# Performance work log

Measured on AMD Instinct MI355X. Metric: run time of the kernel, lower is better.

## Reference

```python
import jax, jax.numpy as jnp
import numpy as np

EMB = 1024
HEADS = 16
FFN = 4096
EPS = 1e-5


def _layernorm(x, g, b):
    mu = jnp.mean(x, axis=-1, keepdims=True)
    var = jnp.mean((x - mu) ** 2, axis=-1, keepdims=True)
    return (x - mu) * jax.lax.rsqrt(var + EPS) * g + b


def setup_inputs() -> dict:
    key = jax.random.key(0)
    ks = jax.random.split(key, 8)
    B, T = 2, 2048
    s_in = 1.0 / np.sqrt(EMB)
    s_ffn = 1.0 / np.sqrt(FFN)
    return {
        "x": jax.random.normal(ks[0], (B, T, EMB), jnp.float32),
        "positions": jnp.arange(B * T, dtype=jnp.int64 if jax.config.jax_enable_x64 else jnp.int32).reshape(B, T),
        "ln1_g": jnp.ones((EMB,), jnp.float32),
        "ln1_b": jnp.zeros((EMB,), jnp.float32),
        "ln2_g": jnp.ones((EMB,), jnp.float32),
        "ln2_b": jnp.zeros((EMB,), jnp.float32),
        "Wq": jax.random.normal(ks[1], (EMB, EMB), jnp.float32) * s_in,
        "bq": jnp.zeros((EMB,), jnp.float32),
        "Wk": jax.random.normal(ks[2], (EMB, EMB), jnp.float32) * s_in,
        "bk": jnp.zeros((EMB,), jnp.float32),
        "Wv": jax.random.normal(ks[3], (EMB, EMB), jnp.float32) * s_in,
        "bv": jnp.zeros((EMB,), jnp.float32),
        "Wo": jax.random.normal(ks[4], (EMB, EMB), jnp.float32) * s_in,
        "bo": jnp.zeros((EMB,), jnp.float32),
        "W1": jax.random.normal(ks[5], (EMB, FFN), jnp.float32) * s_in,
        "b1": jnp.zeros((FFN,), jnp.float32),
        "W2": jax.random.normal(ks[6], (FFN, EMB), jnp.float32) * s_ffn,
        "b2": jnp.zeros((EMB,), jnp.float32),
    }


def reference(x, positions, ln1_g, ln1_b, ln2_g, ln2_b,
              Wq, bq, Wk, bk, Wv, bv, Wo, bo, W1, b1, W2, b2):
    B, T, C = x.shape
    H, D = HEADS, C // HEADS
    # x = ln1(x); then residual branches add onto the normalized x (as in source)
    x = _layernorm(x, ln1_g, ln1_b)
    # --- self attention (rope=None, mask=None, dropout inactive) ---
    q = (x @ Wq + bq).reshape(B, T, H, D).transpose(0, 2, 1, 3)  # [B,H,T,D]
    k = (x @ Wk + bk).reshape(B, T, H, D).transpose(0, 2, 1, 3)
    v = (x @ Wv + bv).reshape(B, T, H, D).transpose(0, 2, 1, 3)
    scale = 1.0 / jnp.sqrt(jnp.asarray(D, x.dtype))
    attn = jnp.einsum("bhtd,bhsd->bhts", q, k) * scale  # [B,H,T,T]
    attn = jax.nn.softmax(attn, axis=-1)
    attn_out = jnp.einsum("bhts,bhsd->bhtd", attn, v)
    attn_out = attn_out.transpose(0, 2, 1, 3).reshape(B, T, C)
    attn_out = attn_out @ Wo + bo
    x = x + attn_out
    # --- FFN with exact (erf) GELU, matching torch nn.GELU default ---
    h = _layernorm(x, ln2_g, ln2_b)
    h = jax.nn.gelu(h @ W1 + b1, approximate=False)
    h = h @ W2 + b2
    return x + h
```

## Files before the change

### kernel.cpp

```cpp
#include <hip/hip_runtime.h>
#include <cstdint>
#include <cstddef>

typedef __bf16 bf16;
typedef __bf16 bf16x8 __attribute__((ext_vector_type(8)));
typedef __bf16 bf16x4 __attribute__((ext_vector_type(4)));
typedef float f32x4 __attribute__((ext_vector_type(4)));

#define TOKENS 4096
#define TSEQ   2048
#define NHEADS 16
#define HDIM   64
#define CDIM   1024

typedef __attribute__((address_space(3))) unsigned int lds_uint;
typedef __attribute__((address_space(1))) const unsigned int g_uint;
__device__ __forceinline__ void glds16(const bf16* g, bf16* l) {
  __builtin_amdgcn_global_load_lds((g_uint*)g, (lds_uint*)l, 16, 0, 0);
}

__device__ __forceinline__ float gelu_f(float v) {
  float g2 = v * (1.5957691216f + 0.0713548163f * v * v);
  return v / (1.0f + __expf(-g2));
}

#define NBUF 17
struct DetectArgs { const void* p[NBUF]; int n[NBUF]; };

__global__ __launch_bounds__(256) void detect_kernel(DetectArgs a, int* __restrict__ flags) {
  __shared__ int s_nz, s_bl;
  if (threadIdx.x == 0) { s_nz = 0; s_bl = 0; }
  __syncthreads();
  int i = blockIdx.x;
  const unsigned int* w = (const unsigned int*)a.p[i];
  int nwords = a.n[i] / 2; if (nwords > 2048) nwords = 2048;
  int nz = 0, bl = 0;
  for (int j = threadIdx.x; j < nwords; j += 256) {
    unsigned int v = w[j];
    if (v != 0u) {
      nz++;
      unsigned int e = (v >> 7) & 0xFFu;
      if (e >= 100u && e <= 140u) bl++;
    }
  }
  atomicAdd(&s_nz, nz);
  atomicAdd(&s_bl, bl);
  __syncthreads();
  if (threadIdx.x == 0) flags[i] = (2 * s_bl >= s_nz) ? 1 : 0;
}

__device__ __forceinline__ float ld_any(const void* p, size_t idx, bool isb) {
  return isb ? (float)((const bf16*)p)[idx] : ((const float*)p)[idx];
}

__device__ __forceinline__ void ln_stats(float s, float s2, int tid, float& mu, float& rstd) {
#pragma unroll
  for (int off = 32; off; off >>= 1) {
    s  += __shfl_down(s, off);
    s2 += __shfl_down(s2, off);
  }
  __shared__ float red[8];
  int w = tid >> 6;
  if ((tid & 63) == 0) { red[w] = s; red[4 + w] = s2; }
  __syncthreads();
  if (tid == 0) {
    red[0] = red[0] + red[1] + red[2] + red[3];
    red[4] = red[4] + red[5] + red[6] + red[7];
  }
  __syncthreads();
  mu = red[0] * (1.0f / CDIM);
  float var = fmaxf(red[4] * (1.0f / CDIM) - mu * mu, 0.f);
  rstd = rsqrtf(var + 1e-5f);
}

__global__ __launch_bounds__(256) void ln_f32(const float* __restrict__ x,
                                              const bf16* __restrict__ g,
                                              const bf16* __restrict__ b,
                                              bf16* __restrict__ y) {
  int row = blockIdx.x, tid = threadIdx.x;
  float v[4]; float s = 0.f, s2 = 0.f;
#pragma unroll
  for (int i = 0; i < 4; i++) {
    float f = x[(size_t)row * CDIM + tid * 4 + i];
    v[i] = f; s += f; s2 += f * f;
  }
  float mu, rstd;
  ln_stats(s, s2, tid, mu, rstd);
  bf16* yr = y + (size_t)row * CDIM;
#pragma unroll
  for (int i = 0; i < 4; i++) {
    int c = tid * 4 + i;
    yr[c] = (bf16)((v[i] - mu) * rstd * (float)g[c] + (float)b[c]);
  }
}

struct MegaArgs {
  const void* w_in[6]; bf16* w_out[6]; int wK[6], wN[6], wflag[6];
  const void* vp[10]; bf16* vd[10]; int vn[10], vfi[10];
  const void* x; const void* graw; const void* braw; bf16* y;
};

__global__ __launch_bounds__(256) void mega_pre(MegaArgs a, const int* __restrict__ flags) {
  int bid = blockIdx.x;
  int tx = threadIdx.x, ty = threadIdx.y;
  int tid = tx + ty * 64;
  if (bid < 3072) {
    __shared__ bf16 tile[64][65];
    int mi, start;
    if (bid < 1024)      { mi = bid >> 8; start = mi << 8; }
    else if (bid < 2048) { mi = 4; start = 1024; }
    else                 { mi = 5; start = 2048; }
    int tb = bid - start;
    int nT = a.wN[mi] >> 6;
    int kb = (tb / nT) * 64, nb = (tb % nT) * 64;
    int K = a.wK[mi], N = a.wN[mi];
    bool isb = flags[a.wflag[mi]] != 0;
    const void* in = a.w_in[mi]; bf16* out = a.w_out[mi];
    for (int i = ty; i < 64; i += 4)
      tile[i][tx] = (bf16)ld_any(in, (size_t)(kb + i) * N + nb + tx, isb);
    __syncthreads();
    for (int i = ty; i < 64; i += 4)
      out[(size_t)(nb + i) * K + kb + tx] = tile[tx][i];
  } else if (bid == 3072) {
    for (int i = 0; i < 10; i++) {
      bool isb = flags[a.vfi[i]] != 0;
      const void* in = a.vp[i]; bf16* out = a.vd[i]; int n = a.vn[i];
      for (int j = tid; j < n; j += 256)
        out[j] = (bf16)ld_any(in, j, isb);
    }
  } else {
    int row = bid - 3073;
    bool isb  = flags[0] != 0;
    bool gisb = flags[1] != 0;
    bool bisb = flags[2] != 0;
    float v[4]; float s = 0.f, s2 = 0.f;
#pragma unroll
    for (int i = 0; i < 4; i++) {
      float f = ld_any(a.x, (size_t)row * CDIM + tid * 4 + i, isb);
      v[i] = f; s += f; s2 += f * f;
    }
    float mu, rstd;
    ln_stats(s, s2, tid, mu, rstd);
    bf16* yr = a.y + (size_t)row * CDIM;
#pragma unroll
    for (int i = 0; i < 4; i++) {
      int c = tid * 4 + i;
      float gv = ld_any(a.graw, c, gisb);
      float bv = ld_any(a.braw, c, bisb);
      yr[c] = (bf16)((v[i] - mu) * rstd * gv + bv);
    }
  }
}

template <int BM, int BN>
__device__ __forceinline__ void gemm_core(const bf16* __restrict__ A,
                                          const bf16* __restrict__ Bt,
                                          int K, int m0, int n0,
                                          bf16* As, bf16* Bs,
                                          f32x4 (&acc)[BM / 32][BN / 32]) {
  constexpr int SI = BM / 32, SJ = BN / 32;
  int t = threadIdx.x;
  int wave = t >> 6, lane = t & 63, quad = lane >> 4, l16 = lane & 15;
  int wm = (wave & 1) * (BM / 2), wn = (wave >> 1) * (BN / 2);
  int srow = t >> 2, sc = t & 3;
  int swz = (srow >> 1) & 3;
  const bf16* ga[BM / 64];
  const bf16* gb[BN / 64];
#pragma unroll
  for (int h = 0; h < BM / 64; h++)
    ga[h] = A + (size_t)(m0 + h * 64 + srow) * K + (sc ^ swz) * 8;
#pragma unroll
  for (int h = 0; h < BN / 64; h++)
    gb[h] = Bt + (size_t)(n0 + h * 64 + srow) * K + (sc ^ swz) * 8;

  for (int k0 = 0; k0 < K; k0 += 64) {
#pragma unroll
    for (int q = 0; q < 2; q++) {
#pragma unroll
      for (int h = 0; h < BM / 64; h++)
        glds16(ga[h] + k0 + q * 32, As + q * (BM * 32) + h * 2048 + srow * 32 + sc * 8);
#pragma unroll
      for (int h = 0; h < BN / 64; h++)
        glds16(gb[h] + k0 + q * 32, Bs + q * (BN * 32) + h * 2048 + srow * 32 + sc * 8);
    }
    __syncthreads();
#pragma unroll
    for (int q = 0; q < 2; q++) {
      bf16x8 af[SI], bfr[SJ];
#pragma unroll
      for (int i = 0; i < SI; i++) {
        int m = wm + i * 16 + l16;
        af[i] = *(const bf16x8*)&As[q * (BM * 32) + m * 32 + ((quad ^ ((m >> 1) & 3)) * 8)];
      }
#pragma unroll
      for (int j = 0; j < SJ; j++) {
        int n = wn + j * 16 + l16;
        bfr[j] = *(const bf16x8*)&Bs[q * (BN * 32) + n * 32 + ((quad ^ ((n >> 1) & 3)) * 8)];
      }
#pragma unroll
      for (int i = 0; i < SI; i++)
#pragma unroll
        for (int j = 0; j < SJ; j++)
          acc[i][j] = __builtin_amdgcn_mfma_f32_16x16x32_bf16(af[i], bfr[j], acc[i][j], 0, 0, 0);
    }
    __syncthreads();
  }
}

#define EPI_NONE 0
#define EPI_RES  1
#define EPI_GELU 2

template <int BM, int BN, int EPI, typename OutT, typename ResT>
__global__ __launch_bounds__(256) void gemm128(const bf16* __restrict__ A,
                                               const bf16* __restrict__ Bt,
                                               const bf16* __restrict__ bias,
                                               const ResT* __restrict__ res,
                                               OutT* __restrict__ C,
                                               int N, int K) {
  __shared__ alignas(16) bf16 As[2 * BM * 32];
  __shared__ alignas(16) bf16 Bs[2 * BN * 32];
  int m0 = blockIdx.y * BM, n0 = blockIdx.x * BN;
  f32x4 acc[BM / 32][BN / 32] = {};
  gemm_core<BM, BN>(A, Bt, K, m0, n0, As, Bs, acc);

  int t = threadIdx.x, wave = t >> 6, lane = t & 63, quad = lane >> 4, l16 = lane & 15;
  int wm = (wave & 1) * (BM / 2), wn = (wave >> 1) * (BN / 2);
#pragma unroll
  for (int i = 0; i < BM / 32; i++)
#pragma unroll
    for (int j = 0; j < BN / 32; j++) {
      int n = n0 + wn + j * 16 + l16;
      float bv = (float)bias[n];
#pragma unroll
      for (int r = 0; r < 4; r++) {
        int m = m0 + wm + i * 16 + quad * 4 + r;
        float v = acc[i][j][r] + bv;
        if (EPI == EPI_GELU)      v = gelu_f(v);
        else if (EPI == EPI_RES)  v += (float)res[(size_t)m * N + n];
        C[(size_t)m * N + n] = (OutT)v;
      }
    }
}

__device__ __forceinline__ void gemm256_core(const bf16* __restrict__ A,
                                             const bf16* __restrict__ Bt,
                                             int K, int m0, int n0,
                                             bf16* sm, f32x4 (&acc)[8][4]) {
  const int NT = K >> 6;
  const int t = threadIdx.x;
  const int lane = t & 63, quad = lane >> 4, l16 = lane & 15;
  const int wave = t >> 6;
  const int wm = (wave & 1) * 128, wn = (wave >> 1) * 64;
  const int srow = t >> 2, sc = t & 3;
  const int swz = (srow >> 1) & 3;
  const int rA = (srow & 63) + ((srow >> 6) << 7);
  const bf16* gA = A + (size_t)(m0 + rA) * K + ((sc ^ swz) << 3);
  const bf16* gB = Bt + (size_t)(n0 + srow) * K + ((sc ^ swz) << 3);
  const int ldsA = rA * 32 + sc * 8;
  const int ldsB = srow * 32 + sc * 8;

  auto stA = [&](int tile, int u) {
    if (tile >= NT) return;
    const bf16* g = gA + (size_t)(u << 6) * K + (tile << 6);
    bf16* l = sm + ((tile & 1) << 15) + ldsA + (u << 11);
    glds16(g, l);
    glds16(g + 32, l + 8192);
  };
  auto stB = [&](int tile, int h) {
    if (tile >= NT) return;
    const bf16* g = gB + (size_t)(h << 7) * K + (tile << 6);
    bf16* l = sm + ((tile & 1) << 15) + 16384 + ldsB + (h << 12);
    glds16(g, l);
    glds16(g + 32, l + 8192);
  };

  stB(0, 0); stB(0, 1); stA(0, 0); stA(0, 1);
  stB(1, 0); stB(1, 1); stA(1, 0);
  asm volatile("s_waitcnt vmcnt(6)" ::: "memory");
  __builtin_amdgcn_s_barrier();
  asm volatile("" ::: "memory");

  bf16x8 bfr[2][4];

#define LDB256(buf)                                                        \
  _Pragma("unroll") for (int q = 0; q < 2; q++)                            \
  _Pragma("unroll") for (int j = 0; j < 4; j++) {                          \
    int nl = wn + j * 16 + l16;                                            \
    bfr[q][j] = *(const bf16x8*)&sm[((buf) << 15) + 16384 + q * 8192 +     \
                                    nl * 32 + ((quad ^ ((nl >> 1) & 3)) << 3)]; \
  }

#define PHASE256(buf, P, STAGE, EXTRAWAIT)                                 \
  {                                                                        \
    bf16x8 af[2][2];                                                       \
    _Pragma("unroll") for (int q = 0; q < 2; q++)                          \
    _Pragma("unroll") for (int i2 = 0; i2 < 2; i2++) {                     \
      int ml = wm + (P) * 32 + i2 * 16 + l16;                              \
      af[q][i2] = *(const bf16x8*)&sm[((buf) << 15) + q * 8192 + ml * 32 + \
                                      ((quad ^ ((ml >> 1) & 3)) << 3)];    \
    }                                                                      \
    if ((P) == 0) { LDB256(buf); }                                         \
    STAGE;                                                                 \
    asm volatile("" ::: "memory");                                         \
    __builtin_amdgcn_s_barrier();                                          \
    asm volatile("s_waitcnt lgkmcnt(0)" ::: "memory");                     \
    __builtin_amdgcn_s_setprio(1);                                         \
    _Pragma("unroll") for (int q = 0; q < 2; q++)                          \
    _Pragma("unroll") for (int i2 = 0; i2 < 2; i2++)                       \
    _Pragma("unroll") for (int j = 0; j < 4; j++)                          \
      acc[(P) * 2 + i2][j] = __builtin_amdgcn_mfma_f32_16x16x32_bf16(      \
          af[q][i2], bfr[q][j], acc[(P) * 2 + i2][j], 0, 0, 0);            \
    __builtin_amdgcn_s_setprio(0);                                         \
    asm volatile("" ::: "memory");                                         \
    EXTRAWAIT;                                                             \
    __builtin_amdgcn_s_barrier();                                          \
    asm volatile("" ::: "memory");                                         \
  }

  for (int t0 = 0; t0 < NT; t0 += 2) {
    const int t1 = t0 + 1;
    PHASE256(0, 0, stA(t1, 1), (void)0);
    PHASE256(0, 1, stB(t0 + 2, 0), (void)0);
    PHASE256(0, 2, stB(t0 + 2, 1), (void)0);
    PHASE256(0, 3, stA(t0 + 2, 0),
             asm volatile("s_waitcnt vmcnt(6)" ::: "memory"));
    PHASE256(1, 0, stA(t0 + 2, 1), (void)0);
    PHASE256(1, 1, stB(t1 + 2, 0), (void)0);
    PHASE256(1, 2, stB(t1 + 2, 1), (void)0);
    PHASE256(1, 3, stA(t1 + 2, 0),
             asm volatile("s_waitcnt vmcnt(6)" ::: "memory"));
  }
#undef PHASE256
#undef LDB256
}

__device__ __forceinline__ void xcd_swizzle(int& bx, int& by) {
  int gx = gridDim.x;
  int nwg = gx * gridDim.y;
  int bid = blockIdx.x + blockIdx.y * gx;
  int wg = (bid & 7) * (nwg >> 3) + (bid >> 3);
  bx = wg % gx; by = wg / gx;
}

__global__ __launch_bounds__(512, 2) void gemm256_gelu(const bf16* __restrict__ A,
                                                       const bf16* __restrict__ Bt,
                                                       const bf16* __restrict__ bias,
                                                       bf16* __restrict__ C,
                                                       int N, int K) {
  __shared__ alignas(16) bf16 sm[65536];
  int bx, by; xcd_swizzle(bx, by);
  int m0 = by * 256, n0 = bx * 256;
  f32x4 acc[8][4] = {};
  gemm256_core(A, Bt, K, m0, n0, sm, acc);

  int t = threadIdx.x, wave = t >> 6, lane = t & 63, quad = lane >> 4, l16 = lane & 15;
  int wm = (wave & 1) * 128, wn = (wave >> 1) * 64;
#pragma unroll
  for (int i = 0; i < 8; i++)
#pragma unroll
    for (int j = 0; j < 4; j++) {
      int n = n0 + wn + j * 16 + l16;
      float bv = (float)bias[n];
#pragma unroll
      for (int r = 0; r < 4; r++) {
        int m = m0 + wm + i * 16 + quad * 4 + r;
        C[(size_t)m * N + n] = (bf16)gelu_f(acc[i][j][r] + bv);
      }
    }
}

__global__ __launch_bounds__(512, 2) void gemm256_qkv(const bf16* __restrict__ A,
                                                      const bf16* __restrict__ Bt,
                                                      const bf16* __restrict__ bias,
                                                      bf16* __restrict__ QK,
                                                      bf16* __restrict__ Vt) {
  __shared__ alignas(16) bf16 sm[65536];
  int bx, by; xcd_swizzle(bx, by);
  int m0 = by * 256, n0 = bx * 256;
  f32x4 acc[8][4] = {};
  gemm256_core(A, Bt, 1024, m0, n0, sm, acc);

  int t = threadIdx.x, wave = t >> 6, lane = t & 63, quad = lane >> 4, l16 = lane & 15;
  int wm = (wave & 1) * 128, wn = (wave >> 1) * 64;
#pragma unroll
  for (int i = 0; i < 8; i++)
#pragma unroll
    for (int j = 0; j < 4; j++) {
      int n = n0 + wn + j * 16 + l16;
      float bv = (float)bias[n];
      int mb = m0 + wm + i * 16 + quad * 4;
      if (n < 1024) {
#pragma unroll
        for (int r = 0; r < 4; r++)
          QK[(size_t)(mb + r) * 2048 + n] = (bf16)((acc[i][j][r] + bv) * 0.125f);
      } else if (n < 2048) {
#pragma unroll
        for (int r = 0; r < 4; r++)
          QK[(size_t)(mb + r) * 2048 + n] = (bf16)(acc[i][j][r] + bv);
      } else {
        bf16x4 pk;
#pragma unroll
        for (int r = 0; r < 4; r++) pk[r] = (bf16)(acc[i][j][r] + bv);
        *(bf16x4*)&Vt[(size_t)(n - 2048) * TOKENS + mb] = pk;
      }
    }
}

__global__ __launch_bounds__(512) void attn_kernel(const bf16* __restrict__ QK,
                                                   const bf16* __restrict__ Vt,
                                                   bf16* __restrict__ O) {
  __shared__ alignas(16) bf16 Ks[2][4096];
  __shared__ alignas(16) bf16 Vs[2][4096];
  __shared__ alignas(16) bf16 Ps[8][16 * 72];
  int b = blockIdx.z, h = blockIdx.y, q0 = blockIdx.x * 128;
  int t = threadIdx.x, wave = t >> 6, lane = t & 63, quad = lane >> 4, l16 = lane & 15;

  const bf16* Qg = QK;
  const bf16* Kg = QK + 1024;
  const size_t bT = (size_t)b * TSEQ;
  const int h64 = h * 64;

  int srow = wave * 8 + (lane >> 3);
  int schunk = (lane & 7) ^ (srow & 7);

  bf16x8 aq0, aq1;
  {
    size_t qrow = bT + q0 + wave * 16 + l16;
    aq0 = *(const bf16x8*)&Qg[qrow * 2048 + h64 + quad * 8];
    aq1 = *(const bf16x8*)&Qg[qrow * 2048 + h64 + 32 + quad * 8];
  }

  f32x4 accO[4] = {};
  f32x4 accL = {};

  auto stage = [&](int tile, int buf) {
    glds16(&Kg[(bT + tile * 64 + srow) * 2048 + h64 + schunk * 8],
           &Ks[buf][wave * 512 + lane * 8]);
    glds16(&Vt[(size_t)(h64 + srow) * TOKENS + bT + tile * 64 + schunk * 8],
           &Vs[buf][wave * 512 + lane * 8]);
  };

  const bf16 one = (bf16)1.0f;
  const bf16x8 onesv = {one, one, one, one, one, one, one, one};
  int sw = l16 & 7;
  bf16* Pw = &Ps[wave][0];

  stage(0, 0);
  __syncthreads();

  for (int it = 0; it < TSEQ / 64; it++) {
    int cur = it & 1;
    if (it + 1 < TSEQ / 64) stage(it + 1, cur ^ 1);

    const bf16* KsC = &Ks[cur][0];
    const bf16* VsC = &Vs[cur][0];

    f32x4 S[4];
#pragma unroll
    for (int c = 0; c < 4; c++) {
      int row = c * 16 + l16;
      bf16x8 kb0 = *(const bf16x8*)&KsC[row * 64 + ((quad ^ sw) * 8)];
      bf16x8 kb1 = *(const bf16x8*)&KsC[row * 64 + (((quad + 4) ^ sw) * 8)];
      f32x4 s = {};
      s = __builtin_amdgcn_mfma_f32_16x16x32_bf16(aq0, kb0, s, 0, 0, 0);
      s = __builtin_amdgcn_mfma_f32_16x16x32_bf16(aq1, kb1, s, 0, 0, 0);
      S[c] = s;
    }

#pragma unroll
    for (int c = 0; c < 4; c++)
#pragma unroll
      for (int r = 0; r < 4; r++)
        Pw[(quad * 4 + r) * 72 + c * 16 + l16] = (bf16)__expf(fminf(S[c][r], 60.f));

    bf16x8 pa0 = *(const bf16x8*)&Pw[l16 * 72 + quad * 8];
    bf16x8 pa1 = *(const bf16x8*)&Pw[l16 * 72 + 32 + quad * 8];
#pragma unroll
    for (int ds = 0; ds < 4; ds++) {
      int row = ds * 16 + l16;
      bf16x8 vb0 = *(const bf16x8*)&VsC[row * 64 + ((quad ^ sw) * 8)];
      bf16x8 vb1 = *(const bf16x8*)&VsC[row * 64 + (((quad + 4) ^ sw) * 8)];
      accO[ds] = __builtin_amdgcn_mfma_f32_16x16x32_bf16(pa0, vb0, accO[ds], 0, 0, 0);
      accO[ds] = __builtin_amdgcn_mfma_f32_16x16x32_bf16(pa1, vb1, accO[ds], 0, 0, 0);
    }
    accL = __builtin_amdgcn_mfma_f32_16x16x32_bf16(pa0, onesv, accL, 0, 0, 0);
    accL = __builtin_amdgcn_mfma_f32_16x16x32_bf16(pa1, onesv, accL, 0, 0, 0);

    __syncthreads();
  }

#pragma unroll
  for (int ds = 0; ds < 4; ds++)
#pragma unroll
    for (int r = 0; r < 4; r++) {
      float v = accO[ds][r] / fmaxf(accL[r], 1e-30f);
      O[(bT + q0 + wave * 16 + quad * 4 + r) * CDIM + h64 + ds * 16 + l16] = (bf16)v;
    }
}

extern "C" void kernel_launch(void* const* d_in, const int* in_sizes, int n_in,
                              void* d_out, int out_size, void* d_ws, size_t ws_size,
                              hipStream_t stream) {
  char* ws = (char*)d_ws;
  const size_t MB = 1024 * 1024;
  const size_t KB = 1024;

  int* flags = (int*)ws;
  bf16* vec_c = (bf16*)(ws + 4 * KB);
  bf16* ln1g_c = vec_c + 0 * 8192;
  bf16* ln1b_c = vec_c + 1 * 8192;
  bf16* ln2g_c = vec_c + 2 * 8192;
  bf16* ln2b_c = vec_c + 3 * 8192;
  bf16* bqkv_c = vec_c + 4 * 8192;
  bf16* bo_c   = vec_c + 6 * 8192;
  bf16* b1_c   = vec_c + 7 * 8192;
  bf16* b2_c   = vec_c + 8 * 8192;

  bf16*  WqkvT  = (bf16*)(ws + 1 * MB);
  bf16*  WoT    = (bf16*)(ws + 7 * MB);
  bf16*  W1T    = (bf16*)(ws + 9 * MB);
  bf16*  W2T    = (bf16*)(ws + 17 * MB);
  bf16*  xn     = (bf16*)(ws + 25 * MB);
  bf16*  QKbuf  = (bf16*)(ws + 33 * MB);
  bf16*  Vtbuf  = (bf16*)(ws + 49 * MB);
  bf16*  ab     = (bf16*)(ws + 57 * MB);
  float* xmid32 = (float*)(ws + 65 * MB);
  bf16*  h2     = (bf16*)(ws + 81 * MB);
  bf16*  f1     = (bf16*)(ws + 33 * MB);

  const int din_idx[NBUF] = {0, 2, 3, 4, 5, 6, 7, 8, 9, 10, 11, 12, 13, 14, 15, 16, 17};
  DetectArgs da;
  for (int i = 0; i < NBUF; i++) { da.p[i] = d_in[din_idx[i]]; da.n[i] = in_sizes[din_idx[i]]; }
  detect_kernel<<<NBUF, 256, 0, stream>>>(da, flags);

  MegaArgs ma;
  {
    const void* wi[6] = {d_in[6], d_in[8], d_in[10], d_in[12], d_in[14], d_in[16]};
    bf16* wo[6] = {WqkvT, WqkvT + 1024 * 1024, WqkvT + 2 * 1024 * 1024, WoT, W1T, W2T};
    const int wK[6] = {1024, 1024, 1024, 1024, 1024, 4096};
    const int wN[6] = {1024, 1024, 1024, 1024, 4096, 1024};
    const int wf[6] = {5, 7, 9, 11, 13, 15};
    for (int i = 0; i < 6; i++) {
      ma.w_in[i] = wi[i]; ma.w_out[i] = wo[i];
      ma.wK[i] = wK[i]; ma.wN[i] = wN[i]; ma.wflag[i] = wf[i];
    }
    const int vf[10] = {1, 2, 3, 4, 6, 8, 10, 12, 14, 16};
    bf16* vd[10] = {ln1g_c, ln1b_c, ln2g_c, ln2b_c,
                    bqkv_c, bqkv_c + 1024, bqkv_c + 2048, bo_c, b1_c, b2_c};
    for (int i = 0; i < 10; i++) {
      int di = din_idx[vf[i]];
      ma.vp[i] = d_in[di]; ma.vd[i] = vd[i]; ma.vn[i] = in_sizes[di]; ma.vfi[i] = vf[i];
    }
    ma.x = d_in[0]; ma.graw = d_in[2]; ma.braw = d_in[3]; ma.y = xn;
  }
  mega_pre<<<3072 + 1 + TOKENS, dim3(64, 4), 0, stream>>>(ma, flags);

  gemm256_qkv<<<dim3(12, 16), 512, 0, stream>>>(xn, WqkvT, bqkv_c, QKbuf, Vtbuf);

  attn_kernel<<<dim3(TSEQ / 128, NHEADS, 2), 512, 0, stream>>>(QKbuf, Vtbuf, ab);

  gemm128<64, 128, EPI_RES, float, bf16><<<dim3(8, 64), 256, 0, stream>>>(
      ab, WoT, bo_c, xn, xmid32, 1024, 1024);

  ln_f32<<<TOKENS, 256, 0, stream>>>(xmid32, ln2g_c, ln2b_c, h2);

  gemm256_gelu<<<dim3(16, 16), 512, 0, stream>>>(h2, W1T, b1_c, f1, 4096, 1024);

  gemm128<64, 128, EPI_RES, float, float><<<dim3(8, 64), 256, 0, stream>>>(
      f1, W2T, b2_c, xmid32, (float*)d_out, 1024, 4096);
}
```

Measured before the change: 384.2 us.

## Rework attention kernel to 32x32x16 MFMA with 4 waves of 32 query rows

Rewrites the attention kernel to use 32x32x16 bf16 MFMAs. Each of 4 waves (256 threads, launch_bounds 256,2) now owns 32 query rows instead of 16. The Q scale folds in log2(e) so the softmax numerator uses exp2f rather than __expf. The P tile layout changes to a swizzled 64-wide buffer and K/V staging issues two loads per thread. The aim is fewer MFMA and LDS instructions per tile and better K/V reuse, at the cost of more registers per wave and fewer waves per block.

```diff
diff --git a/kernel.cpp b/kernel.cpp
--- a/kernel.cpp
+++ b/kernel.cpp
@@ -6,6 +6,7 @@
 typedef __bf16 bf16x8 __attribute__((ext_vector_type(8)));
 typedef __bf16 bf16x4 __attribute__((ext_vector_type(4)));
 typedef float f32x4 __attribute__((ext_vector_type(4)));
+typedef float f32x16 __attribute__((ext_vector_type(16)));
 
 #define TOKENS 4096
 #define TSEQ   2048
@@ -393,7 +394,7 @@
       if (n < 1024) {
 #pragma unroll
         for (int r = 0; r < 4; r++)
-          QK[(size_t)(mb + r) * 2048 + n] = (bf16)((acc[i][j][r] + bv) * 0.125f);
+          QK[(size_t)(mb + r) * 2048 + n] = (bf16)((acc[i][j][r] + bv) * 0.18033688011112042f);
       } else if (n < 2048) {
 #pragma unroll
         for (int r = 0; r < 4; r++)
@@ -407,44 +408,54 @@
     }
 }
 
-__global__ __launch_bounds__(512) void attn_kernel(const bf16* __restrict__ QK,
-                                                   const bf16* __restrict__ Vt,
-                                                   bf16* __restrict__ O) {
+__global__ __launch_bounds__(256, 2) void attn_kernel(const bf16* __restrict__ QK,
+                                                      const bf16* __restrict__ Vt,
+                                                      bf16* __restrict__ O) {
   __shared__ alignas(16) bf16 Ks[2][4096];
   __shared__ alignas(16) bf16 Vs[2][4096];
-  __shared__ alignas(16) bf16 Ps[8][16 * 72];
+  __shared__ alignas(16) bf16 Ps[4][2048];
   int b = blockIdx.z, h = blockIdx.y, q0 = blockIdx.x * 128;
-  int t = threadIdx.x, wave = t >> 6, lane = t & 63, quad = lane >> 4, l16 = lane & 15;
+  int t = threadIdx.x, wave = t >> 6, lane = t & 63;
+  int l31 = lane & 31, l5 = lane >> 5, l7 = lane & 7;
 
   const bf16* Qg = QK;
   const bf16* Kg = QK + 1024;
   const size_t bT = (size_t)b * TSEQ;
   const int h64 = h * 64;
 
-  int srow = wave * 8 + (lane >> 3);
-  int schunk = (lane & 7) ^ (srow & 7);
-
-  bf16x8 aq0, aq1;
+  int sr = lane >> 3;
+  int sch = l7 ^ sr;
+  auto stage = [&](int tile, int buf) {
+    size_t krow = bT + tile * 64 + wave * 8 + sr;
+    bf16* kd = &Ks[buf][wave * 512 + lane * 8];
+    glds16(&Kg[krow * 2048 + h64 + sch * 8], kd);
+    glds16(&Kg[(krow + 32) * 2048 + h64 + sch * 8], kd + 2048);
+    size_t vrow = (size_t)(h64 + wave * 8 + sr) * TOKENS + bT + tile * 64 + sch * 8;
+    bf16* vd = &Vs[buf][wave * 512 + lane * 8];
+    glds16(&Vt[vrow], vd);
+    glds16(&Vt[vrow + (size_t)32 * TOKENS], vd + 2048);
+  };
+
+  bf16x8 qf[4];
   {
-    size_t qrow = bT + q0 + wave * 16 + l16;
-    aq0 = *(const bf16x8*)&Qg[qrow * 2048 + h64 + quad * 8];
-    aq1 = *(const bf16x8*)&Qg[qrow * 2048 + h64 + 32 + quad * 8];
-  }
-
-  f32x4 accO[4] = {};
-  f32x4 accL = {};
-
-  auto stage = [&](int tile, int buf) {
-    glds16(&Kg[(bT + tile * 64 + srow) * 2048 + h64 + schunk * 8],
-           &Ks[buf][wave * 512 + lane * 8]);
-    glds16(&Vt[(size_t)(h64 + srow) * TOKENS + bT + tile * 64 + schunk * 8],
-           &Vs[buf][wave * 512 + lane * 8]);
-  };
-
+    size_t qrow = bT + q0 + wave * 32 + l31;
+    const bf16* qp = &Qg[qrow * 2048 + h64 + l5 * 8];
+#pragma unroll
+    for (int ds = 0; ds < 4; ds++) qf[ds] = *(const bf16x8*)(qp + ds * 16);
+  }
+
+  bf16* PW = &Ps[wave][0];
+  int qb = 4 * l5, c0 = l31 >> 3;
+  int pwb[8];
+#pragma unroll
+  for (int kvt = 0; kvt < 2; kvt++)
+#pragma unroll
+    for (int r3 = 0; r3 < 4; r3++)
+      pwb[kvt * 4 + r3] = (qb + r3) * 64 + (((kvt * 4 + c0) ^ (r3 + qb)) * 8) + l7;
+
+  f32x16 accO0 = {}, accO1 = {}, accL = {};
   const bf16 one = (bf16)1.0f;
   const bf16x8 onesv = {one, one, one, one, one, one, one, one};
-  int sw = l16 & 7;
-  bf16* Pw = &Ps[wave][0];
 
   stage(0, 0);
   __syncthreads();
@@ -456,47 +467,49 @@
     const bf16* KsC = &Ks[cur][0];
     const bf16* VsC = &Vs[cur][0];
 
-    f32x4 S[4];
-#pragma unroll
-    for (int c = 0; c < 4; c++) {
-      int row = c * 16 + l16;
-      bf16x8 kb0 = *(const bf16x8*)&KsC[row * 64 + ((quad ^ sw) * 8)];
-      bf16x8 kb1 = *(const bf16x8*)&KsC[row * 64 + (((quad + 4) ^ sw) * 8)];
-      f32x4 s = {};
-      s = __builtin_amdgcn_mfma_f32_16x16x32_bf16(aq0, kb0, s, 0, 0, 0);
-      s = __builtin_amdgcn_mfma_f32_16x16x32_bf16(aq1, kb1, s, 0, 0, 0);
-      S[c] = s;
-    }
-
-#pragma unroll
-    for (int c = 0; c < 4; c++)
-#pragma unroll
-      for (int r = 0; r < 4; r++)
-        Pw[(quad * 4 + r) * 72 + c * 16 + l16] = (bf16)__expf(fminf(S[c][r], 60.f));
-
-    bf16x8 pa0 = *(const bf16x8*)&Pw[l16 * 72 + quad * 8];
-    bf16x8 pa1 = *(const bf16x8*)&Pw[l16 * 72 + 32 + quad * 8];
+    f32x16 st0 = {}, st1 = {};
 #pragma unroll
     for (int ds = 0; ds < 4; ds++) {
-      int row = ds * 16 + l16;
-      bf16x8 vb0 = *(const bf16x8*)&VsC[row * 64 + ((quad ^ sw) * 8)];
-      bf16x8 vb1 = *(const bf16x8*)&VsC[row * 64 + (((quad + 4) ^ sw) * 8)];
-      accO[ds] = __builtin_amdgcn_mfma_f32_16x16x32_bf16(pa0, vb0, accO[ds], 0, 0, 0);
-      accO[ds] = __builtin_amdgcn_mfma_f32_16x16x32_bf16(pa1, vb1, accO[ds], 0, 0, 0);
-    }
-    accL = __builtin_amdgcn_mfma_f32_16x16x32_bf16(pa0, onesv, accL, 0, 0, 0);
-    accL = __builtin_amdgcn_mfma_f32_16x16x32_bf16(pa1, onesv, accL, 0, 0, 0);
+      int chs = ((ds * 2 + l5) ^ l7) * 8;
+      bf16x8 k0 = *(const bf16x8*)&KsC[l31 * 64 + chs];
+      bf16x8 k1 = *(const bf16x8*)&KsC[(32 + l31) * 64 + chs];
+      st0 = __builtin_amdgcn_mfma_f32_32x32x16_bf16(qf[ds], k0, st0, 0, 0, 0);
+      st1 = __builtin_amdgcn_mfma_f32_32x32x16_bf16(qf[ds], k1, st1, 0, 0, 0);
+    }
+
+#pragma unroll
+    for (int r = 0; r < 16; r++)
+      PW[pwb[r & 3] + (r >> 2) * 512] = (bf16)exp2f(fminf(st0[r], 86.f));
+#pragma unroll
+    for (int r = 0; r < 16; r++)
+      PW[pwb[4 + (r & 3)] + (r >> 2) * 512] = (bf16)exp2f(fminf(st1[r], 86.f));
+
+    bf16x8 pa[4];
+#pragma unroll
+    for (int ks = 0; ks < 4; ks++)
+      pa[ks] = *(const bf16x8*)&PW[l31 * 64 + (((ks * 2 + l5) ^ l7) * 8)];
+
+#pragma unroll
+    for (int ks = 0; ks < 4; ks++) {
+      int chs = ((ks * 2 + l5) ^ l7) * 8;
+      bf16x8 v0 = *(const bf16x8*)&VsC[l31 * 64 + chs];
+      bf16x8 v1 = *(const bf16x8*)&VsC[(32 + l31) * 64 + chs];
+      accO0 = __builtin_amdgcn_mfma_f32_32x32x16_bf16(pa[ks], v0, accO0, 0, 0, 0);
+      accO1 = __builtin_amdgcn_mfma_f32_32x32x16_bf16(pa[ks], v1, accO1, 0, 0, 0);
+      accL  = __builtin_amdgcn_mfma_f32_32x32x16_bf16(pa[ks], onesv, accL, 0, 0, 0);
+    }
 
     __syncthreads();
   }
 
 #pragma unroll
-  for (int ds = 0; ds < 4; ds++)
-#pragma unroll
-    for (int r = 0; r < 4; r++) {
-      float v = accO[ds][r] / fmaxf(accL[r], 1e-30f);
-      O[(bT + q0 + wave * 16 + quad * 4 + r) * CDIM + h64 + ds * 16 + l16] = (bf16)v;
-    }
+  for (int r = 0; r < 16; r++) {
+    int q = (r & 3) + 8 * (r >> 2) + 4 * l5;
+    float rl = 1.0f / fmaxf(accL[r], 1e-30f);
+    size_t orow = (bT + q0 + wave * 32 + q) * CDIM + h64;
+    O[orow + l31]      = (bf16)(accO0[r] * rl);
+    O[orow + 32 + l31] = (bf16)(accO1[r] * rl);
+  }
 }
 
 extern "C" void kernel_launch(void* const* d_in, const int* in_sizes, int n_in,
@@ -558,7 +571,7 @@
 
   gemm256_qkv<<<dim3(12, 16), 512, 0, stream>>>(xn, WqkvT, bqkv_c, QKbuf, Vtbuf);
 
-  attn_kernel<<<dim3(TSEQ / 128, NHEADS, 2), 512, 0, stream>>>(QKbuf, Vtbuf, ab);
+  attn_kernel<<<dim3(TSEQ / 128, NHEADS, 2), 256, 0, stream>>>(QKbuf, Vtbuf, ab);
 
   gemm128<64, 128, EPI_RES, float, bf16><<<dim3(8, 64), 256, 0, stream>>>(
       ab, WoT, bo_c, xn, xmid32, 1024, 1024);
```

Measured after the change: 395.4 us. 1.03x slower.
